# Performance work log

Measured on AMD Instinct MI355X. Metric: run time of the kernel, lower is better.

## Reference

```python
import jax, jax.numpy as jnp
import numpy as np


def setup_inputs() -> dict:
    key = jax.random.key(0)
    k1, k2 = jax.random.split(key)
    n_rows, cols, n_values = 4096, 2048, 16
    x = jax.random.normal(k1, (n_rows, cols), dtype=jnp.float32)
    values = jax.random.normal(k2, (n_rows, n_values), dtype=jnp.float32)
    return {"x": x, "values": values}


def reference(x, values):
    # x: [R, C], values: [R, V] (per-row codebook)
    # distances: [R, C, V] broadcast squared distance
    distances = (x[:, :, None] - values[:, None, :]) ** 2
    min_indices = jnp.argmin(distances, axis=-1)          # [R, C]
    # gather nearest codebook value per row
    selected = jnp.take_along_axis(values, min_indices, axis=1)  # [R, C]
    return selected
```

## Files before the change

### kernel.cpp

```cpp
#include <hip/hip_runtime.h>


#define N_ROWS 4096
#define N_COLS 2048
#define N_VALS 16

typedef float f32x2 __attribute__((ext_vector_type(2)));
typedef float f32x4 __attribute__((ext_vector_type(4)));

static __device__ __forceinline__ float min3f(float a, float b, float c) {
    return fminf(fminf(a, b), c);
}

__global__ __launch_bounds__(256) void vq_rowcodebook_kernel(
    const float* __restrict__ x,
    const float* __restrict__ values,
    float* __restrict__ out)
{
    const int row = blockIdx.x;

    const float* vr = values + (size_t)row * N_VALS;
    float v[N_VALS];
#pragma unroll
    for (int i = 0; i < N_VALS; ++i) v[i] = vr[i];

    const f32x4* xr   = (const f32x4*)(x   + (size_t)row * N_COLS);
    f32x4*       outr = (f32x4*)      (out + (size_t)row * N_COLS);

#pragma unroll
    for (int it = 0; it < 2; ++it) {
        const int j = threadIdx.x + it * 256;
        const f32x4 xv = xr[j];

        f32x4 o;
#pragma unroll
        for (int e = 0; e < 4; ++e) {
            const float xe = xv[e];
            f32x2 xe2; xe2.x = xe; xe2.y = xe;

            float d[N_VALS];
#pragma unroll
            for (int i = 0; i < N_VALS / 2; ++i) {
                f32x2 vv; vv.x = v[2 * i]; vv.y = v[2 * i + 1];
                f32x2 t  = xe2 - vv;
                f32x2 sq = t * t;
                d[2 * i]     = sq.x;
                d[2 * i + 1] = sq.y;
            }

            const float t0 = min3f(d[0],  d[1],  d[2]);
            const float t1 = min3f(d[3],  d[4],  d[5]);
            const float t2 = min3f(d[6],  d[7],  d[8]);
            const float t3 = min3f(d[9],  d[10], d[11]);
            const float t4 = min3f(d[12], d[13], d[14]);
            const float u0 = min3f(t0, t1, t2);
            const float u1 = min3f(t3, t4, d[15]);
            const float md = fminf(u0, u1);

            float bv = v[15];
#pragma unroll
            for (int i = N_VALS - 2; i >= 0; --i)
                bv = (d[i] == md) ? v[i] : bv;

            o[e] = bv;
        }
        outr[j] = o;
    }
}

extern "C" void kernel_launch(void* const* d_in, const int* in_sizes, int n_in,
                              void* d_out, int out_size, void* d_ws, size_t ws_size,
                              hipStream_t stream) {
    const float* x      = (const float*)d_in[0];
    const float* values = (const float*)d_in[1];
    float* out          = (float*)d_out;

    vq_rowcodebook_kernel<<<N_ROWS, 256, 0, stream>>>(x, values, out);
}
```

Before: 86.50 us.

## Replace brute-force codebook scan with sorted-codebook binary search in LDS

Each block first sorts its row's 16 codebook values in shared memory by rank counting, keeping original indices and adding an infinity sentinel. Each element then runs a four-step binary search to find its bracketing pair and picks the nearer of the two, breaking ties by original index. This drops the 16 squared distances, the min tree and the select chain for every element. In exchange it adds a block-wide barrier, a dependent chain of LDS loads per element, and redundant global reads of the codebook during the sort.

```diff
diff --git a/kernel.cpp b/kernel.cpp
--- a/kernel.cpp
+++ b/kernel.cpp
@@ -1,16 +1,14 @@
 #include <hip/hip_runtime.h>
+#include <math.h>
 
 
 #define N_ROWS 4096
 #define N_COLS 2048
 #define N_VALS 16
 
-typedef float f32x2 __attribute__((ext_vector_type(2)));
 typedef float f32x4 __attribute__((ext_vector_type(4)));
 
-static __device__ __forceinline__ float min3f(float a, float b, float c) {
-    return fminf(fminf(a, b), c);
-}
+struct Entry { float v; int idx; };
 
 __global__ __launch_bounds__(256) void vq_rowcodebook_kernel(
     const float* __restrict__ x,
@@ -18,51 +16,57 @@
     float* __restrict__ out)
 {
     const int row = blockIdx.x;
+    const float* vr = values + (size_t)row * N_VALS;
+    const int tid = threadIdx.x;
 
-    const float* vr = values + (size_t)row * N_VALS;
-    float v[N_VALS];
+    __shared__ Entry arr[N_VALS + 1];
+
+    if (tid < N_VALS) {
+        const float vi = vr[tid];
+        int rank = 0;
 #pragma unroll
-    for (int i = 0; i < N_VALS; ++i) v[i] = vr[i];
+        for (int j = 0; j < N_VALS; ++j) {
+            const float vj = vr[j];
+            rank += (vj < vi || (vj == vi && j < tid)) ? 1 : 0;
+        }
+        arr[rank].v = vi;
+        arr[rank].idx = tid;
+        if (tid == 0) { arr[N_VALS].v = INFINITY; arr[N_VALS].idx = 0x7fffffff; }
+    }
+    __syncthreads();
+
+    const float p4 = arr[4].v, p8 = arr[8].v, p12 = arr[12].v;
+    const char* base = (const char*)arr;
 
     const f32x4* xr   = (const f32x4*)(x   + (size_t)row * N_COLS);
     f32x4*       outr = (f32x4*)      (out + (size_t)row * N_COLS);
 
 #pragma unroll
     for (int it = 0; it < 2; ++it) {
-        const int j = threadIdx.x + it * 256;
+        const int j = tid + it * 256;
         const f32x4 xv = xr[j];
 
         f32x4 o;
 #pragma unroll
         for (int e = 0; e < 4; ++e) {
             const float xe = xv[e];
-            f32x2 xe2; xe2.x = xe; xe2.y = xe;
 
-            float d[N_VALS];
-#pragma unroll
-            for (int i = 0; i < N_VALS / 2; ++i) {
-                f32x2 vv; vv.x = v[2 * i]; vv.y = v[2 * i + 1];
-                f32x2 t  = xe2 - vv;
-                f32x2 sq = t * t;
-                d[2 * i]     = sq.x;
-                d[2 * i + 1] = sq.y;
-            }
+            const bool b1 = (p8 <= xe);
+            int posB = b1 ? 64 : 0;
+            const float pv2 = b1 ? p12 : p4;
+            posB += (pv2 <= xe) ? 32 : 0;
+            posB += (*(const float*)(base + posB + 16) <= xe) ? 16 : 0;
+            posB += (*(const float*)(base + posB + 8)  <= xe) ? 8  : 0;
 
-            const float t0 = min3f(d[0],  d[1],  d[2]);
-            const float t1 = min3f(d[3],  d[4],  d[5]);
-            const float t2 = min3f(d[6],  d[7],  d[8]);
-            const float t3 = min3f(d[9],  d[10], d[11]);
-            const float t4 = min3f(d[12], d[13], d[14]);
-            const float u0 = min3f(t0, t1, t2);
-            const float u1 = min3f(t3, t4, d[15]);
-            const float md = fminf(u0, u1);
+            const Entry L = *(const Entry*)(base + posB);
+            const Entry R = *(const Entry*)(base + posB + 8);
 
-            float bv = v[15];
-#pragma unroll
-            for (int i = N_VALS - 2; i >= 0; --i)
-                bv = (d[i] == md) ? v[i] : bv;
-
-            o[e] = bv;
+            const float tL = xe - L.v;
+            const float tR = xe - R.v;
+            const float dL = tL * tL;
+            const float dR = tR * tR;
+            const bool takeL = (dL < dR) | ((dL == dR) & (L.idx < R.idx));
+            o[e] = takeL ? L.v : R.v;
         }
         outr[j] = o;
     }
```

After: 82.88 us. 1.04x faster.
